# Optimization experiments

Measured on AMD Instinct MI355X. Metric: run time of the kernel, lower is better.

## Reference

```python
import jax, jax.numpy as jnp
import numpy as np

FEATURE_DIM = 512
DEPTH = 128
NUM_CLASSES = 1000


def setup_inputs() -> dict:
    key = jax.random.key(0)
    ks = jax.random.split(key, 9)
    s = 1.0 / np.sqrt(FEATURE_DIM)
    sd = 1.0 / np.sqrt(DEPTH)
    return {
        "x": jax.random.normal(ks[0], (8, 2048, FEATURE_DIM), dtype=jnp.float32),
        "Wq": jax.random.uniform(ks[1], (FEATURE_DIM, DEPTH), jnp.float32, -s, s),
        "bq": jax.random.uniform(ks[2], (DEPTH,), jnp.float32, -s, s),
        "Wk": jax.random.uniform(ks[3], (FEATURE_DIM, DEPTH), jnp.float32, -s, s),
        "bk": jax.random.uniform(ks[4], (DEPTH,), jnp.float32, -s, s),
        "Wv": jax.random.uniform(ks[5], (FEATURE_DIM, DEPTH), jnp.float32, -s, s),
        "bv": jax.random.uniform(ks[6], (DEPTH,), jnp.float32, -s, s),
        "Wl": jax.random.uniform(ks[7], (DEPTH, NUM_CLASSES), jnp.float32, -sd, sd),
        "bl": jax.random.uniform(ks[8], (NUM_CLASSES,), jnp.float32, -sd, sd),
    }


def reference(x, Wq, bq, Wk, bk, Wv, bv, Wl, bl):
    # q,k,v: [B,S,depth]
    q = jnp.einsum("bsf,fd->bsd", x, Wq) + bq
    k = jnp.einsum("bsf,fd->bsd", x, Wk) + bk
    v = jnp.einsum("bsf,fd->bsd", x, Wv) + bv
    # NOTE: original applies no 1/sqrt(depth) scaling
    logit = jnp.einsum("bqd,bkd->bqk", q, k)  # [B,S,S]
    attn = jax.nn.softmax(logit, axis=2)
    attn_out = jnp.einsum("bqk,bkd->bqd", attn, v)  # [B,S,depth]
    out = jnp.einsum("bsd,dc->bsc", attn_out, Wl) + bl  # [B,S,C]
    return out.mean(axis=1)  # [B,C]
```

## Files before the change

kernel.cpp:

```cpp
#include <hip/hip_runtime.h>
#include <stdint.h>

#define NB 8
#define SS 2048
#define FF 512
#define DD 128
#define CC 1000
#define KC 8
#define CHUNK (SS / KC)

typedef __attribute__((ext_vector_type(8))) short bf16x8;
typedef __attribute__((ext_vector_type(4))) float f32x4;

__device__ __forceinline__ short f2bf(float f) {
    uint32_t u;
    __builtin_memcpy(&u, &f, 4);
    u = (u + 0x7fffu + ((u >> 16) & 1u)) >> 16;
    return (short)u;
}
__device__ __forceinline__ float bf2f(short h) {
    uint32_t u = ((uint32_t)(uint16_t)h) << 16;
    float f;
    __builtin_memcpy(&f, &u, 4);
    return f;
}
__device__ __forceinline__ void async16(const void* g, void* l) {
    __builtin_amdgcn_global_load_lds(
        (const __attribute__((address_space(1))) uint32_t*)g,
        (__attribute__((address_space(3))) uint32_t*)l, 16, 0, 0);
}

__global__ void prep(const float* __restrict__ x,
                     const float* __restrict__ Wq, const float* __restrict__ Wk,
                     const float* __restrict__ Wv,
                     short* __restrict__ xb, short* __restrict__ Wt)
{
    int bx = blockIdx.x;
    if (bx < 4096) {
        int id = bx * 256 + threadIdx.x;
        const float4* src = (const float4*)x + id * 2;
        float4 a = src[0], b2 = src[1];
        bf16x8 o;
        o[0] = f2bf(a.x);  o[1] = f2bf(a.y);  o[2] = f2bf(a.z);  o[3] = f2bf(a.w);
        o[4] = f2bf(b2.x); o[5] = f2bf(b2.y); o[6] = f2bf(b2.z); o[7] = f2bf(b2.w);
        *(bf16x8*)(xb + id * 8) = o;
    } else {
        int id = (bx - 4096) * 256 + threadIdx.x;
        int w = id >> 16, rem = id & 65535;
        int n = rem >> 9, kx = rem & 511;
        const float* Wsrc = (w == 0) ? Wq : (w == 1) ? Wk : Wv;
        Wt[w * 65536 + n * 512 + kx] = f2bf(Wsrc[kx * 128 + n]);
    }
}

__global__ __launch_bounds__(256) void qkv_proj(
    const short* __restrict__ xb, const short* __restrict__ Wt,
    const float* __restrict__ bq, const float* __restrict__ bk, const float* __restrict__ bv,
    short* __restrict__ qo, short* __restrict__ ko, short* __restrict__ vo)
{
    __shared__ __align__(16) short As[128 * 64];
    __shared__ __align__(16) short Bs[128 * 64];

    const int m0   = blockIdx.x * 128;
    const int mat  = blockIdx.y;
    const int tid  = threadIdx.x;
    const int wave = tid >> 6, lane = tid & 63;
    const int quad = lane >> 4, l16 = lane & 15;
    const int wr = wave >> 1, wc = wave & 1;

    const short* Wm = Wt + mat * 65536;

    f32x4 acc[4][4];
    for (int i = 0; i < 4; i++)
        for (int j = 0; j < 4; j++) acc[i][j] = (f32x4){0.f, 0.f, 0.f, 0.f};

    const int sr = lane >> 3;
    const int sc = (lane & 7) ^ (sr & 7);

    for (int kk = 0; kk < 512; kk += 64) {
        __syncthreads();
        for (int i = 0; i < 4; i++) {
            int ins = wave * 4 + i;
            int r = ins * 8 + sr;
            async16(xb + (m0 + r) * 512 + kk + sc * 8, &As[ins * 512]);
            async16(Wm + r * 512 + kk + sc * 8,        &Bs[ins * 512]);
        }
        __syncthreads();

        for (int kc = 0; kc < 2; kc++) {
            bf16x8 af[4], bfr[4];
            for (int mt = 0; mt < 4; mt++) {
                int R = wr * 64 + mt * 16 + l16, cc = kc * 4 + quad;
                af[mt] = *(const bf16x8*)&As[(R * 8 + (cc ^ (R & 7))) * 8];
            }
            for (int nt = 0; nt < 4; nt++) {
                int R = wc * 64 + nt * 16 + l16, cc = kc * 4 + quad;
                bfr[nt] = *(const bf16x8*)&Bs[(R * 8 + (cc ^ (R & 7))) * 8];
            }
            for (int mt = 0; mt < 4; mt++)
                for (int nt = 0; nt < 4; nt++)
                    acc[mt][nt] = __builtin_amdgcn_mfma_f32_16x16x32_bf16(
                        af[mt], bfr[nt], acc[mt][nt], 0, 0, 0);
        }
    }

    const float* bias = (mat == 0) ? bq : (mat == 1) ? bk : bv;
    short* outp = (mat == 0) ? qo : (mat == 1) ? ko : vo;
    for (int mt = 0; mt < 4; mt++) {
        int grow_base = m0 + wr * 64 + mt * 16 + quad * 4;
        for (int nt = 0; nt < 4; nt++) {
            int col = wc * 64 + nt * 16 + l16;
            float bb = bias[col];
            for (int r = 0; r < 4; r++)
                outp[(grow_base + r) * 128 + col] = f2bf(acc[mt][nt][r] + bb);
        }
    }
}

__global__ __launch_bounds__(256) void attn_l(
    const short* __restrict__ q, const short* __restrict__ k,
    float* __restrict__ l_part, float* __restrict__ accum)
{
    __shared__ __align__(16) short ks[64 * 128];

    const int b  = blockIdx.y;
    const int q0 = blockIdx.x * 128;
    const int lq = blockIdx.z;
    const int c0 = lq * CHUNK;
    const int tid  = threadIdx.x;
    const int wave = tid >> 6, lane = tid & 63;
    const int quad = lane >> 4, l16 = lane & 15;

    if (blockIdx.x == 0 && blockIdx.y == 0 && blockIdx.z == 0) {
        accum[tid] = 0.f; accum[256 + tid] = 0.f;
        accum[512 + tid] = 0.f; accum[768 + tid] = 0.f;
    }

    bf16x8 qf[2][4];
    for (int m = 0; m < 2; m++)
        for (int c = 0; c < 4; c++)
            qf[m][c] = *(const bf16x8*)(q + (b * 2048 + q0 + wave * 32 + m * 16 + l16) * 128
                                          + c * 32 + quad * 8);

    float lsum[2][4] = {{0.f,0.f,0.f,0.f},{0.f,0.f,0.f,0.f}};
    const int krl = lane >> 4;

    for (int s0 = c0; s0 < c0 + CHUNK; s0 += 64) {
        __syncthreads();
        for (int i = 0; i < 4; i++) {
            int ik = wave * 4 + i;
            int kr = ik * 4 + krl;
            int kc8 = (lane & 15) ^ (kr & 15);
            async16(k + (b * 2048 + s0 + kr) * 128 + kc8 * 8, &ks[ik * 512]);
        }
        __syncthreads();

        for (int ct = 0; ct < 4; ct++) {
            f32x4 Sf[2];
            Sf[0] = (f32x4){0.f,0.f,0.f,0.f};
            Sf[1] = (f32x4){0.f,0.f,0.f,0.f};
            int R = ct * 16 + l16;
            for (int c = 0; c < 4; c++) {
                int cc = c * 4 + quad;
                bf16x8 kb = *(const bf16x8*)&ks[(R * 16 + (cc ^ l16)) * 8];
                for (int m = 0; m < 2; m++)
                    Sf[m] = __builtin_amdgcn_mfma_f32_16x16x32_bf16(
                        qf[m][c], kb, Sf[m], 0, 0, 0);
            }
            for (int m = 0; m < 2; m++)
                for (int r = 0; r < 4; r++)
                    lsum[m][r] += __expf(Sf[m][r] - 10.0f);
        }
    }

    for (int m = 0; m < 2; m++)
        for (int r = 0; r < 4; r++) {
            float lv = lsum[m][r];
            lv += __shfl_xor(lv, 1);
            lv += __shfl_xor(lv, 2);
            lv += __shfl_xor(lv, 4);
            lv += __shfl_xor(lv, 8);
            if (l16 == 0)
                l_part[(lq * 8 + b) * 2048 + q0 + wave * 32 + m * 16 + quad * 4 + r] = lv;
        }
}

__global__ __launch_bounds__(256) void attn_w(
    const short* __restrict__ q, const short* __restrict__ k,
    const float* __restrict__ l_part, float* __restrict__ w_part)
{
    __shared__ __align__(16) short ks[64 * 128];
    __shared__ float wl[4][256];

    const int b  = blockIdx.y;
    const int qt = blockIdx.x;
    const int q0 = qt * 128;
    const int lq = blockIdx.z;
    const int c0 = lq * CHUNK;
    const int tid  = threadIdx.x;
    const int wave = tid >> 6, lane = tid & 63;
    const int quad = lane >> 4, l16 = lane & 15;

    bf16x8 qf[2][4];
    for (int m = 0; m < 2; m++)
        for (int c = 0; c < 4; c++)
            qf[m][c] = *(const bf16x8*)(q + (b * 2048 + q0 + wave * 32 + m * 16 + l16) * 128
                                          + c * 32 + quad * 8);

    float linv[2][4];
    for (int m = 0; m < 2; m++)
        for (int r = 0; r < 4; r++) {
            int row = q0 + wave * 32 + m * 16 + quad * 4 + r;
            float lt = 0.f;
            for (int kc = 0; kc < KC; kc++) lt += l_part[(kc * 8 + b) * 2048 + row];
            linv[m][r] = 1.0f / lt;
        }

    const int krl = lane >> 4;

    for (int s0 = c0; s0 < c0 + CHUNK; s0 += 64) {
        __syncthreads();
        for (int i = 0; i < 4; i++) {
            int ik = wave * 4 + i;
            int kr = ik * 4 + krl;
            int kc8 = (lane & 15) ^ (kr & 15);
            async16(k + (b * 2048 + s0 + kr) * 128 + kc8 * 8, &ks[ik * 512]);
        }
        __syncthreads();

        for (int ct = 0; ct < 4; ct++) {
            f32x4 Sf[2];
            Sf[0] = (f32x4){0.f,0.f,0.f,0.f};
            Sf[1] = (f32x4){0.f,0.f,0.f,0.f};
            int R = ct * 16 + l16;
            for (int c = 0; c < 4; c++) {
                int cc = c * 4 + quad;
                bf16x8 kb = *(const bf16x8*)&ks[(R * 16 + (cc ^ l16)) * 8];
                for (int m = 0; m < 2; m++)
                    Sf[m] = __builtin_amdgcn_mfma_f32_16x16x32_bf16(
                        qf[m][c], kb, Sf[m], 0, 0, 0);
            }
            float cs = 0.f;
            for (int m = 0; m < 2; m++)
                for (int r = 0; r < 4; r++)
                    cs += __expf(Sf[m][r] - 10.0f) * linv[m][r];
            cs += __shfl_xor(cs, 16);
            cs += __shfl_xor(cs, 32);
            if (quad == 0) wl[wave][(s0 - c0) + ct * 16 + l16] = cs;
        }
    }

    __syncthreads();
    {
        float s = wl[0][tid] + wl[1][tid] + wl[2][tid] + wl[3][tid];
        w_part[(qt * 8 + b) * 2048 + c0 + tid] = s;
    }
}

__global__ void wv(const float* __restrict__ w_part, const short* __restrict__ vo,
                   float* __restrict__ accum)
{
    __shared__ float wsh[256];
    const int b    = blockIdx.x;
    const int slab = blockIdx.y;
    const int tid  = threadIdx.x;

    int s = slab * 256 + tid;
    float wsum = 0.f;
    for (int qt = 0; qt < 16; qt++) wsum += w_part[(qt * 8 + b) * 2048 + s];
    wsh[tid] = wsum;
    __syncthreads();

    const int d = tid & 127, h = tid >> 7;
    float a = 0.f;
    for (int i = 0; i < 128; i++) {
        int sl = h * 128 + i;
        a += wsh[sl] * bf2f(vo[(size_t)(b * 2048 + slab * 256 + sl) * 128 + d]);
    }
    atomicAdd(&accum[b * 128 + d], a);
}

__global__ void final_proj(const float* __restrict__ accum, const float* __restrict__ Wl,
                           const float* __restrict__ bl, float* __restrict__ out)
{
    int id = blockIdx.x * 256 + threadIdx.x;
    if (id >= NB * CC) return;
    int b = id / CC, c = id % CC;
    float s = 0.f;
    for (int d = 0; d < 128; d++)
        s += accum[b * 128 + d] * Wl[d * 1000 + c];
    out[id] = s * (1.0f / 2048.0f) + bl[c];
}

extern "C" void kernel_launch(void* const* d_in, const int* in_sizes, int n_in,
                              void* d_out, int out_size, void* d_ws, size_t ws_size,
                              hipStream_t stream) {
    const float* x  = (const float*)d_in[0];
    const float* Wq = (const float*)d_in[1];
    const float* bq = (const float*)d_in[2];
    const float* Wk = (const float*)d_in[3];
    const float* bk = (const float*)d_in[4];
    const float* Wv = (const float*)d_in[5];
    const float* bv = (const float*)d_in[6];
    const float* Wl = (const float*)d_in[7];
    const float* bl = (const float*)d_in[8];
    float* out = (float*)d_out;

    char* ws = (char*)d_ws;
    short* qo     = (short*)(ws);
    short* ko     = (short*)(ws + 4194304);
    short* vo     = (short*)(ws + 8388608);
    short* xb     = (short*)(ws + 12582912);
    short* Wt     = (short*)(ws + 29360128);
    float* l_part = (float*)(ws + 29753344);
    float* w_part = (float*)(ws + 30277632);
    float* acc    = (float*)(ws + 31326208);

    prep<<<4864, 256, 0, stream>>>(x, Wq, Wk, Wv, xb, Wt);
    qkv_proj<<<dim3(128, 3), 256, 0, stream>>>(xb, Wt, bq, bk, bv, qo, ko, vo);
    attn_l<<<dim3(16, 8, KC), 256, 0, stream>>>(qo, ko, l_part, acc);
    attn_w<<<dim3(16, 8, KC), 256, 0, stream>>>(qo, ko, l_part, w_part);
    wv<<<dim3(8, 8), 256, 0, stream>>>(w_part, vo, acc);
    final_proj<<<(NB * CC + 255) / 256, 256, 0, stream>>>(acc, Wl, bl, out);
}
```

Before: 152.7 us.

## Double-buffer LDS tiles in QKV and attention kernels, vectorize wv reduction

Adds two-stage LDS double buffering to qkv_proj, attn_l and attn_w so the async load of the next tile is issued before computing on the current one, and drops one barrier per iteration. It also raises wave priority around the MFMA loops. The wv kernel is rewritten to load V eight bf16 at a time and reduce through shared memory, over twice as many blocks. LDS use doubles per block, which may lower occupancy.

```diff
diff --git a/kernel.cpp b/kernel.cpp
--- a/kernel.cpp
+++ b/kernel.cpp
@@ -58,8 +58,8 @@
     const float* __restrict__ bq, const float* __restrict__ bk, const float* __restrict__ bv,
     short* __restrict__ qo, short* __restrict__ ko, short* __restrict__ vo)
 {
-    __shared__ __align__(16) short As[128 * 64];
-    __shared__ __align__(16) short Bs[128 * 64];
+    __shared__ __align__(16) short As[2][128 * 64];
+    __shared__ __align__(16) short Bs[2][128 * 64];
 
     const int m0   = blockIdx.x * 128;
     const int mat  = blockIdx.y;
@@ -77,32 +77,40 @@
     const int sr = lane >> 3;
     const int sc = (lane & 7) ^ (sr & 7);
 
-    for (int kk = 0; kk < 512; kk += 64) {
-        __syncthreads();
-        for (int i = 0; i < 4; i++) {
-            int ins = wave * 4 + i;
-            int r = ins * 8 + sr;
-            async16(xb + (m0 + r) * 512 + kk + sc * 8, &As[ins * 512]);
-            async16(Wm + r * 512 + kk + sc * 8,        &Bs[ins * 512]);
-        }
-        __syncthreads();
+#define QKV_STAGE(buf, kk)                                                  \
+    for (int i = 0; i < 4; i++) {                                           \
+        int ins = wave * 4 + i;                                             \
+        int r = ins * 8 + sr;                                               \
+        async16(xb + (m0 + r) * 512 + (kk) + sc * 8, &As[buf][ins * 512]);  \
+        async16(Wm + r * 512 + (kk) + sc * 8,        &Bs[buf][ins * 512]);  \
+    }
+
+    QKV_STAGE(0, 0)
+    __syncthreads();
+
+    int cur = 0;
+    for (int t = 0; t < 8; t++) {
+        if (t < 7) { QKV_STAGE(cur ^ 1, (t + 1) * 64) }
 
         for (int kc = 0; kc < 2; kc++) {
             bf16x8 af[4], bfr[4];
             for (int mt = 0; mt < 4; mt++) {
                 int R = wr * 64 + mt * 16 + l16, cc = kc * 4 + quad;
-                af[mt] = *(const bf16x8*)&As[(R * 8 + (cc ^ (R & 7))) * 8];
+                af[mt] = *(const bf16x8*)&As[cur][(R * 8 + (cc ^ (R & 7))) * 8];
             }
             for (int nt = 0; nt < 4; nt++) {
                 int R = wc * 64 + nt * 16 + l16, cc = kc * 4 + quad;
-                bfr[nt] = *(const bf16x8*)&Bs[(R * 8 + (cc ^ (R & 7))) * 8];
+                bfr[nt] = *(const bf16x8*)&Bs[cur][(R * 8 + (cc ^ (R & 7))) * 8];
             }
             for (int mt = 0; mt < 4; mt++)
                 for (int nt = 0; nt < 4; nt++)
                     acc[mt][nt] = __builtin_amdgcn_mfma_f32_16x16x32_bf16(
                         af[mt], bfr[nt], acc[mt][nt], 0, 0, 0);
         }
-    }
+        __syncthreads();
+        cur ^= 1;
+    }
+#undef QKV_STAGE
 
     const float* bias = (mat == 0) ? bq : (mat == 1) ? bk : bv;
     short* outp = (mat == 0) ? qo : (mat == 1) ? ko : vo;
@@ -121,7 +129,7 @@
     const short* __restrict__ q, const short* __restrict__ k,
     float* __restrict__ l_part, float* __restrict__ accum)
 {
-    __shared__ __align__(16) short ks[64 * 128];
+    __shared__ __align__(16) short ks[2][64 * 128];
 
     const int b  = blockIdx.y;
     const int q0 = blockIdx.x * 128;
@@ -145,32 +153,41 @@
     float lsum[2][4] = {{0.f,0.f,0.f,0.f},{0.f,0.f,0.f,0.f}};
     const int krl = lane >> 4;
 
-    for (int s0 = c0; s0 < c0 + CHUNK; s0 += 64) {
-        __syncthreads();
-        for (int i = 0; i < 4; i++) {
-            int ik = wave * 4 + i;
-            int kr = ik * 4 + krl;
-            int kc8 = (lane & 15) ^ (kr & 15);
-            async16(k + (b * 2048 + s0 + kr) * 128 + kc8 * 8, &ks[ik * 512]);
-        }
-        __syncthreads();
+#define K_STAGE(buf, s0)                                                     \
+    for (int i = 0; i < 4; i++) {                                            \
+        int ik = wave * 4 + i;                                               \
+        int kr = ik * 4 + krl;                                               \
+        int kc8 = (lane & 15) ^ (kr & 15);                                   \
+        async16(k + (b * 2048 + (s0) + kr) * 128 + kc8 * 8, &ks[buf][ik * 512]); \
+    }
+
+    K_STAGE(0, c0)
+    __syncthreads();
+
+    int cur = 0;
+    for (int t = 0; t < CHUNK / 64; t++) {
+        if (t < CHUNK / 64 - 1) { K_STAGE(cur ^ 1, c0 + (t + 1) * 64) }
 
         for (int ct = 0; ct < 4; ct++) {
             f32x4 Sf[2];
             Sf[0] = (f32x4){0.f,0.f,0.f,0.f};
             Sf[1] = (f32x4){0.f,0.f,0.f,0.f};
             int R = ct * 16 + l16;
+            __builtin_amdgcn_s_setprio(1);
             for (int c = 0; c < 4; c++) {
                 int cc = c * 4 + quad;
-                bf16x8 kb = *(const bf16x8*)&ks[(R * 16 + (cc ^ l16)) * 8];
+                bf16x8 kb = *(const bf16x8*)&ks[cur][(R * 16 + (cc ^ l16)) * 8];
                 for (int m = 0; m < 2; m++)
                     Sf[m] = __builtin_amdgcn_mfma_f32_16x16x32_bf16(
                         qf[m][c], kb, Sf[m], 0, 0, 0);
             }
+            __builtin_amdgcn_s_setprio(0);
             for (int m = 0; m < 2; m++)
                 for (int r = 0; r < 4; r++)
                     lsum[m][r] += __expf(Sf[m][r] - 10.0f);
         }
+        __syncthreads();
+        cur ^= 1;
     }
 
     for (int m = 0; m < 2; m++)
@@ -189,7 +206,7 @@
     const short* __restrict__ q, const short* __restrict__ k,
     const float* __restrict__ l_part, float* __restrict__ w_part)
 {
-    __shared__ __align__(16) short ks[64 * 128];
+    __shared__ __align__(16) short ks[2][64 * 128];
     __shared__ float wl[4][256];
 
     const int b  = blockIdx.y;
@@ -218,28 +235,28 @@
 
     const int krl = lane >> 4;
 
-    for (int s0 = c0; s0 < c0 + CHUNK; s0 += 64) {
-        __syncthreads();
-        for (int i = 0; i < 4; i++) {
-            int ik = wave * 4 + i;
-            int kr = ik * 4 + krl;
-            int kc8 = (lane & 15) ^ (kr & 15);
-            async16(k + (b * 2048 + s0 + kr) * 128 + kc8 * 8, &ks[ik * 512]);
-        }
-        __syncthreads();
+    K_STAGE(0, c0)
+    __syncthreads();
+
+    int cur = 0;
+    for (int t = 0; t < CHUNK / 64; t++) {
+        if (t < CHUNK / 64 - 1) { K_STAGE(cur ^ 1, c0 + (t + 1) * 64) }
+        int s0 = c0 + t * 64;
 
         for (int ct = 0; ct < 4; ct++) {
             f32x4 Sf[2];
             Sf[0] = (f32x4){0.f,0.f,0.f,0.f};
             Sf[1] = (f32x4){0.f,0.f,0.f,0.f};
             int R = ct * 16 + l16;
+            __builtin_amdgcn_s_setprio(1);
             for (int c = 0; c < 4; c++) {
                 int cc = c * 4 + quad;
-                bf16x8 kb = *(const bf16x8*)&ks[(R * 16 + (cc ^ l16)) * 8];
+                bf16x8 kb = *(const bf16x8*)&ks[cur][(R * 16 + (cc ^ l16)) * 8];
                 for (int m = 0; m < 2; m++)
                     Sf[m] = __builtin_amdgcn_mfma_f32_16x16x32_bf16(
                         qf[m][c], kb, Sf[m], 0, 0, 0);
             }
+            __builtin_amdgcn_s_setprio(0);
             float cs = 0.f;
             for (int m = 0; m < 2; m++)
                 for (int r = 0; r < 4; r++)
@@ -248,36 +265,52 @@
             cs += __shfl_xor(cs, 32);
             if (quad == 0) wl[wave][(s0 - c0) + ct * 16 + l16] = cs;
         }
-    }
-
-    __syncthreads();
+        __syncthreads();
+        cur ^= 1;
+    }
+#undef K_STAGE
+
     {
         float s = wl[0][tid] + wl[1][tid] + wl[2][tid] + wl[3][tid];
         w_part[(qt * 8 + b) * 2048 + c0 + tid] = s;
     }
 }
 
-__global__ void wv(const float* __restrict__ w_part, const short* __restrict__ vo,
-                   float* __restrict__ accum)
-{
-    __shared__ float wsh[256];
+__global__ __launch_bounds__(256) void wv(
+    const float* __restrict__ w_part, const short* __restrict__ vo,
+    float* __restrict__ accum)
+{
+    __shared__ float wsh[128];
+    __shared__ float red[16][129];
     const int b    = blockIdx.x;
     const int slab = blockIdx.y;
     const int tid  = threadIdx.x;
 
-    int s = slab * 256 + tid;
-    float wsum = 0.f;
-    for (int qt = 0; qt < 16; qt++) wsum += w_part[(qt * 8 + b) * 2048 + s];
-    wsh[tid] = wsum;
-    __syncthreads();
-
-    const int d = tid & 127, h = tid >> 7;
-    float a = 0.f;
-    for (int i = 0; i < 128; i++) {
-        int sl = h * 128 + i;
-        a += wsh[sl] * bf2f(vo[(size_t)(b * 2048 + slab * 256 + sl) * 128 + d]);
-    }
-    atomicAdd(&accum[b * 128 + d], a);
+    if (tid < 128) {
+        int s = slab * 128 + tid;
+        float wsum = 0.f;
+        for (int qt = 0; qt < 16; qt++) wsum += w_part[(qt * 8 + b) * 2048 + s];
+        wsh[tid] = wsum;
+    }
+    __syncthreads();
+
+    const int dgrp = tid & 15, sgrp = tid >> 4;
+    const int d0 = dgrp * 8;
+    float a[8] = {0.f,0.f,0.f,0.f,0.f,0.f,0.f,0.f};
+    for (int i = 0; i < 8; i++) {
+        int sl = sgrp * 8 + i;
+        bf16x8 v = *(const bf16x8*)(vo + (size_t)(b * 2048 + slab * 128 + sl) * 128 + d0);
+        float w = wsh[sl];
+        for (int j = 0; j < 8; j++) a[j] += w * bf2f(v[j]);
+    }
+    for (int j = 0; j < 8; j++) red[sgrp][d0 + j] = a[j];
+    __syncthreads();
+
+    if (tid < 128) {
+        float s = 0.f;
+        for (int g = 0; g < 16; g++) s += red[g][tid];
+        atomicAdd(&accum[b * 128 + tid], s);
+    }
 }
 
 __global__ void final_proj(const float* __restrict__ accum, const float* __restrict__ Wl,
@@ -320,6 +353,6 @@
     qkv_proj<<<dim3(128, 3), 256, 0, stream>>>(xb, Wt, bq, bk, bv, qo, ko, vo);
     attn_l<<<dim3(16, 8, KC), 256, 0, stream>>>(qo, ko, l_part, acc);
     attn_w<<<dim3(16, 8, KC), 256, 0, stream>>>(qo, ko, l_part, w_part);
-    wv<<<dim3(8, 8), 256, 0, stream>>>(w_part, vo, acc);
+    wv<<<dim3(8, 16), 256, 0, stream>>>(w_part, vo, acc);
     final_proj<<<(NB * CC + 255) / 256, 256, 0, stream>>>(acc, Wl, bl, out);
 }
```

After: 148.6 us. -2.7%, faster.
